# Kernel optimization log

Hardware: AMD Instinct MI355X
Metric: run time of the kernel (lower is better)

## Reference

```python
import jax, jax.numpy as jnp
import numpy as np

NUM_FEATURES = 1_000_000  # np.max(999999)+1
EMBED_DIM = 64
NUM_FIELDS = 39
BATCH = 16384


def setup_inputs() -> dict:
    key = jax.random.key(0)
    k_x, k_e, k_b, k_w = jax.random.split(key, 4)
    x = jax.random.randint(k_x, (BATCH, NUM_FIELDS), 0, NUM_FEATURES, dtype=jnp.int64 if jax.config.jax_enable_x64 else jnp.int32)
    # trunc_normal_(std=0.01) ~ small normal init; plain normal*0.01 is fine for a numeric reference
    embeddings = jax.random.normal(k_e, (NUM_FEATURES, EMBED_DIM), dtype=jnp.float32) * 0.01
    bias = jax.random.normal(k_b, (NUM_FEATURES, 1), dtype=jnp.float32) * 0.01
    field_inter_weights = jax.random.normal(k_w, (NUM_FIELDS, NUM_FIELDS), dtype=jnp.float32) * 0.01
    w0 = jnp.zeros((1,), dtype=jnp.float32)
    return {"x": x, "embeddings": embeddings, "bias": bias,
            "field_inter_weights": field_inter_weights, "w0": w0}


def reference(x, embeddings, bias, field_inter_weights, w0):
    # emb: (B, F, D) gathered rows
    emb = embeddings[x]
    # bias lookup -> (B, F), summed over fields
    biases_sum = bias[x][..., 0].sum(axis=1)  # (B,)
    # zero the diagonal of the field interaction weight matrix
    W = field_inter_weights - jnp.diag(jnp.diag(field_inter_weights))  # (F, F)
    # batched Gram matrix emb @ emb^T : (B, F, F)
    gram = jnp.einsum('bid,bjd->bij', emb, emb)
    inter = 0.5 * jnp.einsum('bij,ij->b', gram, W)  # weighted sum over both field dims
    return w0 + biases_sum + inter  # (B,)
```

## Files before the change

kernel.cpp:

```cpp
#include <hip/hip_runtime.h>


constexpr int NF = 39;
constexpr int D  = 64;
constexpr int NPAIR = NF * (NF - 1) / 2;
constexpr int WAVES_PER_BLOCK = 4;
constexpr int NT = 64 * WAVES_PER_BLOCK;

__global__ __launch_bounds__(256) void prep_w(const float* __restrict__ W,
                                              float* __restrict__ P) {
    int t = blockIdx.x * blockDim.x + threadIdx.x;
    if (t >= NPAIR) return;
    int j = (int)((1.0f + sqrtf(1.0f + 8.0f * (float)t)) * 0.5f);
    while (j > 1 && j * (j - 1) / 2 > t) --j;
    while ((j + 1) * j / 2 <= t) ++j;
    int i = t - j * (j - 1) / 2;
    P[t] = 0.5f * (W[i * NF + j] + W[j * NF + i]);
}

__global__ __launch_bounds__(NT) void fwfm_kernel(
    const int*   __restrict__ x,
    const float* __restrict__ emb,
    const float* __restrict__ bias,
    const float* __restrict__ P,
    const float* __restrict__ w0,
    float*       __restrict__ out)
{
    const int lane = threadIdx.x & 63;
    const int wave = __builtin_amdgcn_readfirstlane((int)(threadIdx.x >> 6));
    const int b    = blockIdx.x * WAVES_PER_BLOCK + wave;

    const int* xrow = x + (size_t)b * NF;

    int idx[NF];
    #pragma unroll
    for (int f = 0; f < NF; ++f) idx[f] = xrow[f];

    float E[NF];
    #pragma unroll
    for (int f = 0; f < NF; ++f)
        E[f] = emb[(size_t)idx[f] * D + lane];

    float bsum = 0.0f;
    #pragma unroll
    for (int f = 0; f < NF; ++f) bsum += bias[idx[f]];

    float q = 0.0f;
    #pragma unroll
    for (int j = 1; j < NF; ++j) {
        const int base = j * (j - 1) / 2;
        float s0 = 0.0f, s1 = 0.0f;
        #pragma unroll
        for (int i = 0; i + 1 < j; i += 2) {
            s0 = fmaf(P[base + i],     E[i],     s0);
            s1 = fmaf(P[base + i + 1], E[i + 1], s1);
        }
        if (j & 1) s0 = fmaf(P[base + j - 1], E[j - 1], s0);
        q = fmaf(E[j], s0 + s1, q);
    }

    #pragma unroll
    for (int off = 32; off > 0; off >>= 1)
        q += __shfl_down(q, off, 64);

    if (lane == 0)
        out[b] = w0[0] + bsum + q;
}

extern "C" void kernel_launch(void* const* d_in, const int* in_sizes, int n_in,
                              void* d_out, int out_size, void* d_ws, size_t ws_size,
                              hipStream_t stream) {
    const int*   x    = (const int*)d_in[0];
    const float* emb  = (const float*)d_in[1];
    const float* bias = (const float*)d_in[2];
    const float* W    = (const float*)d_in[3];
    const float* w0   = (const float*)d_in[4];
    float*       out  = (float*)d_out;
    float*       P    = (float*)d_ws;

    prep_w<<<(NPAIR + 255) / 256, 256, 0, stream>>>(W, P);

    const int batch = out_size;
    fwfm_kernel<<<batch / WAVES_PER_BLOCK, NT, 0, stream>>>(x, emb, bias, P, w0, out);
}
```

Measured before the change: 353.5 us.

## Fuse pair-weight prep into main kernel via LDS and parallelize bias gather

Removes the separate prep_w launch. Each block now builds the symmetrized pair-weight table in shared memory from W before the main computation, and reads it from LDS instead of global memory. The bias lookup is also spread across lanes, with one field per lane, and folded into the existing wave reduction. This replaces 39 serial bias loads per lane. In exchange, every block recomputes the 741-entry table and waits at a __syncthreads barrier.

```diff
diff --git a/kernel.cpp b/kernel.cpp
--- a/kernel.cpp
+++ b/kernel.cpp
@@ -7,30 +7,34 @@
 constexpr int WAVES_PER_BLOCK = 4;
 constexpr int NT = 64 * WAVES_PER_BLOCK;
 
-__global__ __launch_bounds__(256) void prep_w(const float* __restrict__ W,
-                                              float* __restrict__ P) {
-    int t = blockIdx.x * blockDim.x + threadIdx.x;
-    if (t >= NPAIR) return;
-    int j = (int)((1.0f + sqrtf(1.0f + 8.0f * (float)t)) * 0.5f);
-    while (j > 1 && j * (j - 1) / 2 > t) --j;
-    while ((j + 1) * j / 2 <= t) ++j;
-    int i = t - j * (j - 1) / 2;
-    P[t] = 0.5f * (W[i * NF + j] + W[j * NF + i]);
-}
-
 __global__ __launch_bounds__(NT) void fwfm_kernel(
     const int*   __restrict__ x,
     const float* __restrict__ emb,
     const float* __restrict__ bias,
-    const float* __restrict__ P,
+    const float* __restrict__ W,
     const float* __restrict__ w0,
     float*       __restrict__ out)
 {
+    __shared__ float Pl[NPAIR];
+
+    for (int t = threadIdx.x; t < NPAIR; t += NT) {
+        int j = (int)((1.0f + sqrtf(1.0f + 8.0f * (float)t)) * 0.5f);
+        while (j > 1 && j * (j - 1) / 2 > t) --j;
+        while ((j + 1) * j / 2 <= t) ++j;
+        int i = t - j * (j - 1) / 2;
+        Pl[t] = 0.5f * (W[i * NF + j] + W[j * NF + i]);
+    }
+
+    __syncthreads();
+
     const int lane = threadIdx.x & 63;
     const int wave = __builtin_amdgcn_readfirstlane((int)(threadIdx.x >> 6));
     const int b    = blockIdx.x * WAVES_PER_BLOCK + wave;
 
     const int* xrow = x + (size_t)b * NF;
+
+    float bv = 0.0f;
+    if (lane < NF) bv = bias[xrow[lane]];
 
     int idx[NF];
     #pragma unroll
@@ -41,10 +45,6 @@
     for (int f = 0; f < NF; ++f)
         E[f] = emb[(size_t)idx[f] * D + lane];
 
-    float bsum = 0.0f;
-    #pragma unroll
-    for (int f = 0; f < NF; ++f) bsum += bias[idx[f]];
-
     float q = 0.0f;
     #pragma unroll
     for (int j = 1; j < NF; ++j) {
@@ -52,19 +52,20 @@
         float s0 = 0.0f, s1 = 0.0f;
         #pragma unroll
         for (int i = 0; i + 1 < j; i += 2) {
-            s0 = fmaf(P[base + i],     E[i],     s0);
-            s1 = fmaf(P[base + i + 1], E[i + 1], s1);
+            s0 = fmaf(Pl[base + i],     E[i],     s0);
+            s1 = fmaf(Pl[base + i + 1], E[i + 1], s1);
         }
-        if (j & 1) s0 = fmaf(P[base + j - 1], E[j - 1], s0);
+        if (j & 1) s0 = fmaf(Pl[base + j - 1], E[j - 1], s0);
         q = fmaf(E[j], s0 + s1, q);
     }
 
+    float v = q + bv;
     #pragma unroll
     for (int off = 32; off > 0; off >>= 1)
-        q += __shfl_down(q, off, 64);
+        v += __shfl_down(v, off, 64);
 
     if (lane == 0)
-        out[b] = w0[0] + bsum + q;
+        out[b] = w0[0] + v;
 }
 
 extern "C" void kernel_launch(void* const* d_in, const int* in_sizes, int n_in,
@@ -76,10 +77,8 @@
     const float* W    = (const float*)d_in[3];
     const float* w0   = (const float*)d_in[4];
     float*       out  = (float*)d_out;
-    float*       P    = (float*)d_ws;
-
-    prep_w<<<(NPAIR + 255) / 256, 256, 0, stream>>>(W, P);
+    (void)d_ws; (void)ws_size;
 
     const int batch = out_size;
-    fwfm_kernel<<<batch / WAVES_PER_BLOCK, NT, 0, stream>>>(x, emb, bias, P, w0, out);
+    fwfm_kernel<<<batch / WAVES_PER_BLOCK, NT, 0, stream>>>(x, emb, bias, W, w0, out);
 }
```

Result: faster. 328.2 us (-7.1%).
